# Kernel optimization log

Hardware: AMD Instinct MI355X
Metric: run time of the kernel (lower is better)

## Reference

```python
import jax, jax.numpy as jnp
import numpy as np

NUM_HEAD = 8


def setup_inputs() -> dict:
    key = jax.random.key(0)
    ks = jax.random.split(key, 8)
    B, N, M, C, R = 4, 2048, 2048, 256, 128
    s = 1.0 / np.sqrt(C)
    return {
        "input_q": jax.random.normal(ks[0], (B, N, C), jnp.float32),
        "input_k": jax.random.normal(ks[1], (B, M, C), jnp.float32),
        "input_v": jax.random.normal(ks[2], (B, M, C), jnp.float32),
        "rpe_indices": jax.random.randint(ks[3], (B, N, M), 0, R, jnp.int32),
        "key_masks": jnp.zeros((B, M), jnp.float32),
        "Wq": jax.random.normal(ks[4], (C, C), jnp.float32) * s,
        "bq": jnp.zeros((C,), jnp.float32),
        "Wk": jax.random.normal(ks[5], (C, C), jnp.float32) * s,
        "bk": jnp.zeros((C,), jnp.float32),
        "Wv": jax.random.normal(ks[6], (C, C), jnp.float32) * s,
        "bv": jnp.zeros((C,), jnp.float32),
        "rpe_bank": jax.random.normal(ks[7], (R, C), jnp.float32),
    }


def reference(input_q, input_k, input_v, rpe_indices, key_masks,
              Wq, bq, Wk, bk, Wv, bv, rpe_bank):
    B, N, C = input_q.shape
    M = input_k.shape[1]
    H = NUM_HEAD
    Dh = C // H
    R = rpe_bank.shape[0]

    # projections -> (B, H, len, Dh)
    q = (input_q @ Wq + bq).reshape(B, N, H, Dh).transpose(0, 2, 1, 3)
    k = (input_k @ Wk + bk).reshape(B, M, H, Dh).transpose(0, 2, 1, 3)
    v = (input_v @ Wv + bv).reshape(B, M, H, Dh).transpose(0, 2, 1, 3)

    # RPE bank split per head: (H, R, Dh)
    rpe = rpe_bank.reshape(R, H, Dh).transpose(1, 0, 2)

    # q . rpe for all bins, then gather per (n, m) relative index
    scores_p_all = jnp.einsum('bhnd,hrd->bhnr', q, rpe)            # (B,H,N,R)
    idx = jnp.broadcast_to(rpe_indices[:, None, :, :], (B, H, N, M))
    scores_p = jnp.take_along_axis(scores_p_all, idx, axis=-1)     # (B,H,N,M)

    scores_e = jnp.einsum('bhnd,bhmd->bhnm', q, k)                 # (B,H,N,M)
    scores = (scores_e + scores_p) / jnp.sqrt(jnp.asarray(Dh, q.dtype))
    scores = scores + key_masks[:, None, None, :]

    attn = jax.nn.softmax(scores, axis=-1)
    out = jnp.einsum('bhnm,bhmd->bhnd', attn, v)                   # (B,H,N,Dh)
    return out.transpose(0, 2, 1, 3).reshape(B, N, C)
```

## Files before the change

### kernel.cpp

```cpp
#include <hip/hip_runtime.h>
#include <hip/hip_bf16.h>

#define B_ 4
#define N_ 2048
#define M_ 2048
#define C_ 256
#define H_ 8
#define DH_ 32
#define R_ 128

typedef __bf16 bf16x8 __attribute__((ext_vector_type(8)));
typedef float f32x4 __attribute__((ext_vector_type(4)));

#define QSCL 0.25503486f
#define LOG2E 1.4426950408889634f
#define DTHR 11.5f

#define GLOAD_LDS4(gp, lp)                                            \
    __builtin_amdgcn_global_load_lds(                                 \
        (const __attribute__((address_space(1))) void*)(gp),          \
        (__attribute__((address_space(3))) void*)(lp), 4, 0, 0)

__global__ __launch_bounds__(256) void wtrans_kernel(
    const float* __restrict__ Wq, const float* __restrict__ Wk,
    const float* __restrict__ Wv, __bf16* __restrict__ out)
{
    __shared__ float t[32][33];
    int pz = blockIdx.z;
    const float* W = pz == 0 ? Wq : (pz == 1 ? Wk : Wv);
    int j0 = blockIdx.x * 32, k0 = blockIdx.y * 32;
    int tx = threadIdx.x, ty = threadIdx.y;
#pragma unroll
    for (int i = 0; i < 4; ++i)
        t[ty + 8 * i][tx] = W[(k0 + ty + 8 * i) * C_ + j0 + tx];
    __syncthreads();
    __bf16* o = out + (size_t)pz * C_ * C_;
#pragma unroll
    for (int i = 0; i < 4; ++i)
        o[(j0 + ty + 8 * i) * C_ + k0 + tx] = (__bf16)t[tx][ty + 8 * i];
}

__global__ __launch_bounds__(256) void proj_kernel(
    const float* __restrict__ Xq, const float* __restrict__ Xk, const float* __restrict__ Xv,
    const float* __restrict__ bq, const float* __restrict__ bk, const float* __restrict__ bv,
    const __bf16* __restrict__ Wt,
    __bf16* __restrict__ qb, __bf16* __restrict__ kb, __bf16* __restrict__ vt)
{
    int pz = blockIdx.z;
    const float* X = pz == 0 ? Xq : (pz == 1 ? Xk : Xv);
    const float* bias = pz == 0 ? bq : (pz == 1 ? bk : bv);
    const __bf16* W = Wt + (size_t)pz * C_ * C_;

    int r0 = blockIdx.x * 64;
    int w = threadIdx.x >> 6, lane = threadIdx.x & 63;
    int lg = lane >> 4, lr = lane & 15;
    int rw = r0 + w * 16;

    f32x4 z = {0.f, 0.f, 0.f, 0.f};
    f32x4 acc[16];
#pragma unroll
    for (int ns = 0; ns < 16; ++ns) acc[ns] = z;

    for (int ks = 0; ks < 8; ++ks) {
        const float* ap = X + (size_t)(rw + lr) * C_ + ks * 32 + lg * 8;
        float4 a0 = *(const float4*)ap;
        float4 a1 = *(const float4*)(ap + 4);
        bf16x8 af;
        af[0] = (__bf16)a0.x; af[1] = (__bf16)a0.y; af[2] = (__bf16)a0.z; af[3] = (__bf16)a0.w;
        af[4] = (__bf16)a1.x; af[5] = (__bf16)a1.y; af[6] = (__bf16)a1.z; af[7] = (__bf16)a1.w;
        if (pz < 2) {
#pragma unroll
            for (int ns = 0; ns < 16; ++ns) {
                bf16x8 bfv = *(const bf16x8*)(W + (size_t)(ns * 16 + lr) * C_ + ks * 32 + lg * 8);
                acc[ns] = __builtin_amdgcn_mfma_f32_16x16x32_bf16(bfv, af, acc[ns], 0, 0, 0);
            }
        } else {
#pragma unroll
            for (int ns = 0; ns < 16; ++ns) {
                bf16x8 bfv = *(const bf16x8*)(W + (size_t)(ns * 16 + lr) * C_ + ks * 32 + lg * 8);
                acc[ns] = __builtin_amdgcn_mfma_f32_16x16x32_bf16(af, bfv, acc[ns], 0, 0, 0);
            }
        }
    }

    if (pz < 2) {
        int ng = rw + lr;
        int bb = ng >> 11, n = ng & (N_ - 1);
        unsigned short* dst = (unsigned short*)(pz == 0 ? qb : kb);
#pragma unroll
        for (int ns = 0; ns < 16; ++ns) {
            int j0b = ns * 16 + 4 * lg;
            float4 b4 = *(const float4*)(bias + j0b);
            int hh = j0b >> 5, d0 = j0b & 31;
            float v0 = acc[ns][0] + b4.x, v1 = acc[ns][1] + b4.y;
            float v2 = acc[ns][2] + b4.z, v3 = acc[ns][3] + b4.w;
            if (pz == 0) { v0 *= QSCL; v1 *= QSCL; v2 *= QSCL; v3 *= QSCL; }
            ushort4 pk;
            pk.x = __builtin_bit_cast(unsigned short, (__bf16)v0);
            pk.y = __builtin_bit_cast(unsigned short, (__bf16)v1);
            pk.z = __builtin_bit_cast(unsigned short, (__bf16)v2);
            pk.w = __builtin_bit_cast(unsigned short, (__bf16)v3);
            *(ushort4*)(dst + ((((size_t)bb * H_ + hh) * 2048 + n) * DH_ + d0)) = pk;
        }
    } else {
        int r = rw + lg * 4;
        int bb = r >> 11, n = r & (N_ - 1);
#pragma unroll
        for (int ns = 0; ns < 16; ++ns) {
            int j = ns * 16 + lr;
            float bj = bias[j];
            int hh = j >> 5, d = j & 31;
            ushort4 pk;
            pk.x = __builtin_bit_cast(unsigned short, (__bf16)(acc[ns][0] + bj));
            pk.y = __builtin_bit_cast(unsigned short, (__bf16)(acc[ns][1] + bj));
            pk.z = __builtin_bit_cast(unsigned short, (__bf16)(acc[ns][2] + bj));
            pk.w = __builtin_bit_cast(unsigned short, (__bf16)(acc[ns][3] + bj));
            *(ushort4*)((unsigned short*)vt + (((size_t)bb * H_ + hh) * DH_ + d) * M_ + n) = pk;
        }
    }
}

__global__ __launch_bounds__(512) void attn_kernel(
    const __bf16* __restrict__ qb, const __bf16* __restrict__ kb,
    const __bf16* __restrict__ vt, const int* __restrict__ ridx,
    const float* __restrict__ kmask, const float* __restrict__ rbank,
    float* __restrict__ out)
{
    __shared__ __bf16 Pall[H_][16][R_];
    __shared__ int idxS[2][16 * 64];

    int lin = blockIdx.x;
    int b = (lin & 7) >> 1;
    int xq = ((lin >> 3) << 1) | (lin & 1);
    int n0 = xq * 16;

    int h = threadIdx.x >> 6, lane = threadIdx.x & 63;
    int lg = lane >> 4, lr = lane & 15;
    f32x4 z = {0.f, 0.f, 0.f, 0.f};

    const int* ixblk = ridx + ((size_t)b * N_ + n0) * M_;

#pragma unroll
    for (int i = 0; i < 2; ++i) {
        int r = 2 * h + i;
        int sw = 4 * (r & 7);
        GLOAD_LDS4(ixblk + (size_t)r * M_ + (lane ^ sw), &idxS[0][r * 64]);
    }

    bf16x8 qf = *(const bf16x8*)(qb + (((size_t)b * H_ + h) * N_ + n0 + lr) * DH_ + lg * 8);

    for (int rs = 0; rs < R_ / 16; ++rs) {
        const float* rp = rbank + (size_t)(rs * 16 + lr) * C_ + h * DH_ + lg * 8;
        float4 r0v = *(const float4*)rp;
        float4 r1v = *(const float4*)(rp + 4);
        bf16x8 rf;
        rf[0] = (__bf16)r0v.x; rf[1] = (__bf16)r0v.y; rf[2] = (__bf16)r0v.z; rf[3] = (__bf16)r0v.w;
        rf[4] = (__bf16)r1v.x; rf[5] = (__bf16)r1v.y; rf[6] = (__bf16)r1v.z; rf[7] = (__bf16)r1v.w;
        f32x4 pc = __builtin_amdgcn_mfma_f32_16x16x32_bf16(qf, rf, z, 0, 0, 0);
#pragma unroll
        for (int reg = 0; reg < 4; ++reg)
            Pall[h][lg * 4 + reg][rs * 16 + lr] = (__bf16)pc[reg];
    }

    __syncthreads();

    const __bf16* Kh = kb + ((size_t)b * H_ + h) * M_ * DH_;
    const __bf16* Vh = vt + ((size_t)b * H_ + h) * DH_ * M_;
    const float* km = kmask + (size_t)b * M_;
    const __bf16* PallR = &Pall[h][lr][0];
    int swzR = 4 * (lr & 7);

    float mrow = -1e30f, lrun = 0.f;
    f32x4 acc[2] = {z, z};
    int cb = 0;

    for (int mt = 0; mt < M_ / 64; ++mt) {
        int m0 = mt * 64;
        int m0n = (mt < 31) ? m0 + 64 : m0;

#pragma unroll
        for (int i = 0; i < 2; ++i) {
            int r = 2 * h + i;
            int sw = 4 * (r & 7);
            GLOAD_LDS4(ixblk + (size_t)r * M_ + m0n + (lane ^ sw), &idxS[cb ^ 1][r * 64]);
        }

        bf16x8 kf[4];
#pragma unroll
        for (int ms = 0; ms < 4; ++ms)
            kf[ms] = *(const bf16x8*)(Kh + (size_t)(m0 + ms * 16 + lr) * DH_ + lg * 8);
        bf16x8 vf[4];
#pragma unroll
        for (int ds = 0; ds < 2; ++ds)
#pragma unroll
            for (int ks = 0; ks < 2; ++ks)
                vf[ds * 2 + ks] = *(const bf16x8*)(Vh + (size_t)(ds * 16 + lr) * M_ + m0 + ks * 32 + lg * 8);
        float4 mkv[4];
#pragma unroll
        for (int ms = 0; ms < 4; ++ms)
            mkv[ms] = *(const float4*)(km + m0 + ms * 16 + 4 * lg);

        int4 ixv[4];
#pragma unroll
        for (int ms = 0; ms < 4; ++ms)
            ixv[ms] = *(const int4*)&idxS[cb][lr * 64 + ((16 * ms + 4 * lg) ^ swzR)];
        float sv[16];
#pragma unroll
        for (int ms = 0; ms < 4; ++ms) {
            sv[ms * 4 + 0] = (float)PallR[ixv[ms].x];
            sv[ms * 4 + 1] = (float)PallR[ixv[ms].y];
            sv[ms * 4 + 2] = (float)PallR[ixv[ms].z];
            sv[ms * 4 + 3] = (float)PallR[ixv[ms].w];
        }

        f32x4 st[4];
#pragma unroll
        for (int ms = 0; ms < 4; ++ms)
            st[ms] = __builtin_amdgcn_mfma_f32_16x16x32_bf16(kf[ms], qf, z, 0, 0, 0);

#pragma unroll
        for (int ms = 0; ms < 4; ++ms) {
            sv[ms * 4 + 0] = fmaf(mkv[ms].x, LOG2E, st[ms][0] + sv[ms * 4 + 0]);
            sv[ms * 4 + 1] = fmaf(mkv[ms].y, LOG2E, st[ms][1] + sv[ms * 4 + 1]);
            sv[ms * 4 + 2] = fmaf(mkv[ms].z, LOG2E, st[ms][2] + sv[ms * 4 + 2]);
            sv[ms * 4 + 3] = fmaf(mkv[ms].w, LOG2E, st[ms][3] + sv[ms * 4 + 3]);
        }

        float pmax = sv[0];
#pragma unroll
        for (int j = 1; j < 16; ++j) pmax = fmaxf(pmax, sv[j]);
        pmax = fmaxf(pmax, __shfl_xor(pmax, 16));
        pmax = fmaxf(pmax, __shfl_xor(pmax, 32));

        if (!__all(pmax - mrow <= DTHR)) {
            float mnew = fmaxf(mrow, pmax);
            float alpha = exp2f(mrow - mnew);
            mrow = mnew;
            lrun *= alpha;
#pragma unroll
            for (int reg = 0; reg < 4; ++reg) {
                float aB = __shfl(alpha, lg * 4 + reg);
                acc[0][reg] *= aB;
                acc[1][reg] *= aB;
            }
        }

        float pq[16], ssum = 0.f;
#pragma unroll
        for (int j = 0; j < 16; ++j) {
            pq[j] = exp2f(sv[j] - mrow);
            ssum += pq[j];
        }
        ssum += __shfl_xor(ssum, 16);
        ssum += __shfl_xor(ssum, 32);
        lrun += ssum;

        unsigned int pw[8];
#pragma unroll
        for (int p = 0; p < 8; ++p) {
            unsigned int lo = __builtin_bit_cast(unsigned short, (__bf16)pq[2 * p]);
            unsigned int hi = __builtin_bit_cast(unsigned short, (__bf16)pq[2 * p + 1]);
            pw[p] = lo | (hi << 16);
        }
        bool hiHalf = lane >= 32;
#pragma unroll
        for (int ks = 0; ks < 2; ++ks) {
            uint4 wv;
            unsigned int* wp = (unsigned int*)&wv;
#pragma unroll
            for (int wi = 0; wi < 4; ++wi) {
                int src = (((2 * lg + (wi >> 1)) & 3) << 4) + lr;
                unsigned int a0 = __shfl(pw[4 * ks + (wi & 1)], src);
                unsigned int a1 = __shfl(pw[4 * ks + 2 + (wi & 1)], src);
                wp[wi] = hiHalf ? a1 : a0;
            }
            bf16x8 pf = __builtin_bit_cast(bf16x8, wv);
#pragma unroll
            for (int ds = 0; ds < 2; ++ds)
                acc[ds] = __builtin_amdgcn_mfma_f32_16x16x32_bf16(pf, vf[ds * 2 + ks], acc[ds], 0, 0, 0);
        }

        __syncthreads();
        cb ^= 1;
    }

#pragma unroll
    for (int reg = 0; reg < 4; ++reg) {
        float lB = __shfl(lrun, lg * 4 + reg);
        float inv = 1.0f / lB;
        size_t rb = ((size_t)b * N_ + n0 + lg * 4 + reg) * C_ + h * DH_;
        out[rb + lr] = acc[0][reg] * inv;
        out[rb + 16 + lr] = acc[1][reg] * inv;
    }
}

extern "C" void kernel_launch(void* const* d_in, const int* in_sizes, int n_in,
                              void* d_out, int out_size, void* d_ws, size_t ws_size,
                              hipStream_t stream) {
    const float* Xq = (const float*)d_in[0];
    const float* Xk = (const float*)d_in[1];
    const float* Xv = (const float*)d_in[2];
    const int* ridx = (const int*)d_in[3];
    const float* kmask = (const float*)d_in[4];
    const float* Wq = (const float*)d_in[5];
    const float* bq = (const float*)d_in[6];
    const float* Wk = (const float*)d_in[7];
    const float* bk = (const float*)d_in[8];
    const float* Wv = (const float*)d_in[9];
    const float* bv = (const float*)d_in[10];
    const float* rbank = (const float*)d_in[11];
    float* outp = (float*)d_out;

    char* ws = (char*)d_ws;
    __bf16* Wt = (__bf16*)ws;
    __bf16* qb = (__bf16*)(ws + 393216);
    __bf16* kb = (__bf16*)(ws + 393216 + 4194304);
    __bf16* vt = (__bf16*)(ws + 393216 + 8388608);

    wtrans_kernel<<<dim3(8, 8, 3), dim3(32, 8), 0, stream>>>(Wq, Wk, Wv, Wt);
    proj_kernel<<<dim3(128, 1, 3), 256, 0, stream>>>(Xq, Xk, Xv, bq, bk, bv, Wt, qb, kb, vt);
    attn_kernel<<<512, 512, 0, stream>>>(qb, kb, vt, ridx, kmask, rbank, outp);
}
```

Before: 168.2 us.

## Split attention over key halves with a merge kernel and fast exp2

```diff
diff --git a/kernel.cpp b/kernel.cpp
--- a/kernel.cpp
+++ b/kernel.cpp
@@ -15,6 +15,12 @@
 #define QSCL 0.25503486f
 #define LOG2E 1.4426950408889634f
 #define DTHR 11.5f
+
+__device__ __forceinline__ float fast_exp2(float x) {
+    float r;
+    asm("v_exp_f32 %0, %1" : "=v"(r) : "v"(x));
+    return r;
+}
 
 #define GLOAD_LDS4(gp, lp)                                            \
     __builtin_amdgcn_global_load_lds(                                 \
@@ -120,19 +126,21 @@
     }
 }
 
-__global__ __launch_bounds__(512) void attn_kernel(
+__global__ __launch_bounds__(512, 8) void attn_kernel(
     const __bf16* __restrict__ qb, const __bf16* __restrict__ kb,
     const __bf16* __restrict__ vt, const int* __restrict__ ridx,
     const float* __restrict__ kmask, const float* __restrict__ rbank,
-    float* __restrict__ out)
+    float* __restrict__ Opart, float* __restrict__ Ms, float* __restrict__ Ls)
 {
     __shared__ __bf16 Pall[H_][16][R_];
     __shared__ int idxS[2][16 * 64];
 
     int lin = blockIdx.x;
+    int mh = lin & 1;
     int b = (lin & 7) >> 1;
-    int xq = ((lin >> 3) << 1) | (lin & 1);
+    int xq = lin >> 3;
     int n0 = xq * 16;
+    int mbase = mh * (M_ / 2);
 
     int h = threadIdx.x >> 6, lane = threadIdx.x & 63;
     int lg = lane >> 4, lr = lane & 15;
@@ -144,7 +152,7 @@
     for (int i = 0; i < 2; ++i) {
         int r = 2 * h + i;
         int sw = 4 * (r & 7);
-        GLOAD_LDS4(ixblk + (size_t)r * M_ + (lane ^ sw), &idxS[0][r * 64]);
+        GLOAD_LDS4(ixblk + (size_t)r * M_ + mbase + (lane ^ sw), &idxS[0][r * 64]);
     }
 
     bf16x8 qf = *(const bf16x8*)(qb + (((size_t)b * H_ + h) * N_ + n0 + lr) * DH_ + lg * 8);
@@ -174,9 +182,9 @@
     f32x4 acc[2] = {z, z};
     int cb = 0;
 
-    for (int mt = 0; mt < M_ / 64; ++mt) {
-        int m0 = mt * 64;
-        int m0n = (mt < 31) ? m0 + 64 : m0;
+    for (int mt = 0; mt < 16; ++mt) {
+        int m0 = mbase + mt * 64;
+        int m0n = (mt < 15) ? m0 + 64 : m0;
 
 #pragma unroll
         for (int i = 0; i < 2; ++i) {
@@ -234,7 +242,7 @@
 
         if (!__all(pmax - mrow <= DTHR)) {
             float mnew = fmaxf(mrow, pmax);
-            float alpha = exp2f(mrow - mnew);
+            float alpha = fast_exp2(mrow - mnew);
             mrow = mnew;
             lrun *= alpha;
 #pragma unroll
@@ -248,7 +256,7 @@
         float pq[16], ssum = 0.f;
 #pragma unroll
         for (int j = 0; j < 16; ++j) {
-            pq[j] = exp2f(sv[j] - mrow);
+            pq[j] = fast_exp2(sv[j] - mrow);
             ssum += pq[j];
         }
         ssum += __shfl_xor(ssum, 16);
@@ -284,14 +292,49 @@
         cb ^= 1;
     }
 
+    float* Op = Opart + ((((size_t)mh * B_ + b) * N_ + n0)) * C_ + h * DH_;
 #pragma unroll
     for (int reg = 0; reg < 4; ++reg) {
-        float lB = __shfl(lrun, lg * 4 + reg);
-        float inv = 1.0f / lB;
-        size_t rb = ((size_t)b * N_ + n0 + lg * 4 + reg) * C_ + h * DH_;
-        out[rb + lr] = acc[0][reg] * inv;
-        out[rb + 16 + lr] = acc[1][reg] * inv;
-    }
+        size_t rb = (size_t)(4 * lg + reg) * C_;
+        Op[rb + lr] = acc[0][reg];
+        Op[rb + 16 + lr] = acc[1][reg];
+    }
+    if (lane < 16) {
+        size_t si = (((size_t)mh * B_ + b) * H_ + h) * N_ + n0 + lr;
+        Ms[si] = mrow;
+        Ls[si] = lrun;
+    }
+}
+
+__global__ __launch_bounds__(256) void merge_kernel(
+    const float* __restrict__ Opart, const float* __restrict__ Ms,
+    const float* __restrict__ Ls, float* __restrict__ out)
+{
+    int t = blockIdx.x * 256 + threadIdx.x;
+    int c4 = t & 63;
+    int n = (t >> 6) & (N_ - 1);
+    int bb = t >> 17;
+    int h = c4 >> 3;
+
+    size_t s0 = ((size_t)bb * H_ + h) * N_ + n;
+    size_t s1 = (((size_t)B_ + bb) * H_ + h) * N_ + n;
+    float m0 = Ms[s0], m1 = Ms[s1];
+    float l0 = Ls[s0], l1 = Ls[s1];
+    float mm = fmaxf(m0, m1);
+    float w0 = fast_exp2(m0 - mm), w1 = fast_exp2(m1 - mm);
+    float inv = 1.0f / (l0 * w0 + l1 * w1);
+    w0 *= inv; w1 *= inv;
+
+    size_t o0i = ((size_t)bb * N_ + n) * C_ + c4 * 4;
+    size_t o1i = (((size_t)B_ + bb) * N_ + n) * C_ + c4 * 4;
+    float4 o0 = *(const float4*)(Opart + o0i);
+    float4 o1 = *(const float4*)(Opart + o1i);
+    float4 r;
+    r.x = o0.x * w0 + o1.x * w1;
+    r.y = o0.y * w0 + o1.y * w1;
+    r.z = o0.z * w0 + o1.z * w1;
+    r.w = o0.w * w0 + o1.w * w1;
+    *(float4*)(out + ((size_t)bb * N_ + n) * C_ + c4 * 4) = r;
 }
 
 extern "C" void kernel_launch(void* const* d_in, const int* in_sizes, int n_in,
@@ -316,8 +359,12 @@
     __bf16* qb = (__bf16*)(ws + 393216);
     __bf16* kb = (__bf16*)(ws + 393216 + 4194304);
     __bf16* vt = (__bf16*)(ws + 393216 + 8388608);
+    float* Opart = (float*)(ws + 12976128);
+    float* Msb = (float*)(ws + 12976128 + 16777216);
+    float* Lsb = (float*)(ws + 12976128 + 16777216 + 524288);
 
     wtrans_kernel<<<dim3(8, 8, 3), dim3(32, 8), 0, stream>>>(Wq, Wk, Wv, Wt);
     proj_kernel<<<dim3(128, 1, 3), 256, 0, stream>>>(Xq, Xk, Xv, bq, bk, bv, Wt, qb, kb, vt);
-    attn_kernel<<<512, 512, 0, stream>>>(qb, kb, vt, ridx, kmask, rbank, outp);
-}
+    attn_kernel<<<1024, 512, 0, stream>>>(qb, kb, vt, ridx, kmask, rbank, Opart, Msb, Lsb);
+    merge_kernel<<<2048, 256, 0, stream>>>(Opart, Msb, Lsb, outp);
+}
```

Measured after the change: 207.0 us. 1.23x slower.

## Permute V layout to drop P shuffles, prefetch K, defer row-sum reduction

Applied to the files above, without the earlier changes.

```diff
diff --git a/kernel.cpp b/kernel.cpp
--- a/kernel.cpp
+++ b/kernel.cpp
@@ -15,6 +15,12 @@
 #define QSCL 0.25503486f
 #define LOG2E 1.4426950408889634f
 #define DTHR 11.5f
+
+__device__ __forceinline__ float fast_exp2(float x) {
+    float r;
+    asm("v_exp_f32 %0, %1" : "=v"(r) : "v"(x));
+    return r;
+}
 
 #define GLOAD_LDS4(gp, lp)                                            \
     __builtin_amdgcn_global_load_lds(                                 \
@@ -105,6 +111,7 @@
     } else {
         int r = rw + lg * 4;
         int bb = r >> 11, n = r & (N_ - 1);
+        int np = (n & ~31) | (((n >> 2) & 3) << 3) | (((n >> 4) & 1) << 2);
 #pragma unroll
         for (int ns = 0; ns < 16; ++ns) {
             int j = ns * 16 + lr;
@@ -115,12 +122,12 @@
             pk.y = __builtin_bit_cast(unsigned short, (__bf16)(acc[ns][1] + bj));
             pk.z = __builtin_bit_cast(unsigned short, (__bf16)(acc[ns][2] + bj));
             pk.w = __builtin_bit_cast(unsigned short, (__bf16)(acc[ns][3] + bj));
-            *(ushort4*)((unsigned short*)vt + (((size_t)bb * H_ + hh) * DH_ + d) * M_ + n) = pk;
-        }
-    }
-}
-
-__global__ __launch_bounds__(512) void attn_kernel(
+            *(ushort4*)((unsigned short*)vt + (((size_t)bb * H_ + hh) * DH_ + d) * M_ + np) = pk;
+        }
+    }
+}
+
+__global__ __launch_bounds__(512, 4) void attn_kernel(
     const __bf16* __restrict__ qb, const __bf16* __restrict__ kb,
     const __bf16* __restrict__ vt, const int* __restrict__ ridx,
     const float* __restrict__ kmask, const float* __restrict__ rbank,
@@ -162,18 +169,24 @@
             Pall[h][lg * 4 + reg][rs * 16 + lr] = (__bf16)pc[reg];
     }
 
-    __syncthreads();
-
     const __bf16* Kh = kb + ((size_t)b * H_ + h) * M_ * DH_;
     const __bf16* Vh = vt + ((size_t)b * H_ + h) * DH_ * M_;
     const float* km = kmask + (size_t)b * M_;
     const __bf16* PallR = &Pall[h][lr][0];
     int swzR = 4 * (lr & 7);
 
-    float mrow = -1e30f, lrun = 0.f;
+    bf16x8 kf[4];
+#pragma unroll
+    for (int ms = 0; ms < 4; ++ms)
+        kf[ms] = *(const bf16x8*)(Kh + (size_t)(ms * 16 + lr) * DH_ + lg * 8);
+
+    __syncthreads();
+
+    float mrow = -1e30f, lloc = 0.f;
     f32x4 acc[2] = {z, z};
     int cb = 0;
 
+#pragma unroll 2
     for (int mt = 0; mt < M_ / 64; ++mt) {
         int m0 = mt * 64;
         int m0n = (mt < 31) ? m0 + 64 : m0;
@@ -185,10 +198,11 @@
             GLOAD_LDS4(ixblk + (size_t)r * M_ + m0n + (lane ^ sw), &idxS[cb ^ 1][r * 64]);
         }
 
-        bf16x8 kf[4];
+        bf16x8 kf_n[4];
 #pragma unroll
         for (int ms = 0; ms < 4; ++ms)
-            kf[ms] = *(const bf16x8*)(Kh + (size_t)(m0 + ms * 16 + lr) * DH_ + lg * 8);
+            kf_n[ms] = *(const bf16x8*)(Kh + (size_t)(m0n + ms * 16 + lr) * DH_ + lg * 8);
+
         bf16x8 vf[4];
 #pragma unroll
         for (int ds = 0; ds < 2; ++ds)
@@ -226,17 +240,19 @@
             sv[ms * 4 + 3] = fmaf(mkv[ms].w, LOG2E, st[ms][3] + sv[ms * 4 + 3]);
         }
 
-        float pmax = sv[0];
-#pragma unroll
-        for (int j = 1; j < 16; ++j) pmax = fmaxf(pmax, sv[j]);
-        pmax = fmaxf(pmax, __shfl_xor(pmax, 16));
-        pmax = fmaxf(pmax, __shfl_xor(pmax, 32));
+        float t0 = fmaxf(fmaxf(sv[0], sv[1]), fmaxf(sv[2], sv[3]));
+        float t1 = fmaxf(fmaxf(sv[4], sv[5]), fmaxf(sv[6], sv[7]));
+        float t2 = fmaxf(fmaxf(sv[8], sv[9]), fmaxf(sv[10], sv[11]));
+        float t3 = fmaxf(fmaxf(sv[12], sv[13]), fmaxf(sv[14], sv[15]));
+        float pmax = fmaxf(fmaxf(t0, t1), fmaxf(t2, t3));
 
         if (!__all(pmax - mrow <= DTHR)) {
-            float mnew = fmaxf(mrow, pmax);
-            float alpha = exp2f(mrow - mnew);
+            float rmax = fmaxf(pmax, __shfl_xor(pmax, 16));
+            rmax = fmaxf(rmax, __shfl_xor(rmax, 32));
+            float mnew = fmaxf(mrow, rmax);
+            float alpha = fast_exp2(mrow - mnew);
             mrow = mnew;
-            lrun *= alpha;
+            lloc *= alpha;
 #pragma unroll
             for (int reg = 0; reg < 4; ++reg) {
                 float aB = __shfl(alpha, lg * 4 + reg);
@@ -245,36 +261,22 @@
             }
         }
 
-        float pq[16], ssum = 0.f;
-#pragma unroll
-        for (int j = 0; j < 16; ++j) {
-            pq[j] = exp2f(sv[j] - mrow);
-            ssum += pq[j];
-        }
-        ssum += __shfl_xor(ssum, 16);
-        ssum += __shfl_xor(ssum, 32);
-        lrun += ssum;
-
-        unsigned int pw[8];
-#pragma unroll
-        for (int p = 0; p < 8; ++p) {
-            unsigned int lo = __builtin_bit_cast(unsigned short, (__bf16)pq[2 * p]);
-            unsigned int hi = __builtin_bit_cast(unsigned short, (__bf16)pq[2 * p + 1]);
-            pw[p] = lo | (hi << 16);
-        }
-        bool hiHalf = lane >= 32;
+        float pq[16];
+#pragma unroll
+        for (int j = 0; j < 16; ++j) pq[j] = fast_exp2(sv[j] - mrow);
+        {
+            float s0 = (pq[0] + pq[1]) + (pq[2] + pq[3]);
+            float s1 = (pq[4] + pq[5]) + (pq[6] + pq[7]);
+            float s2 = (pq[8] + pq[9]) + (pq[10] + pq[11]);
+            float s3 = (pq[12] + pq[13]) + (pq[14] + pq[15]);
+            lloc += (s0 + s1) + (s2 + s3);
+        }
+
 #pragma unroll
         for (int ks = 0; ks < 2; ++ks) {
-            uint4 wv;
-            unsigned int* wp = (unsigned int*)&wv;
-#pragma unroll
-            for (int wi = 0; wi < 4; ++wi) {
-                int src = (((2 * lg + (wi >> 1)) & 3) << 4) + lr;
-                unsigned int a0 = __shfl(pw[4 * ks + (wi & 1)], src);
-                unsigned int a1 = __shfl(pw[4 * ks + 2 + (wi & 1)], src);
-                wp[wi] = hiHalf ? a1 : a0;
-            }
-            bf16x8 pf = __builtin_bit_cast(bf16x8, wv);
+            bf16x8 pf;
+#pragma unroll
+            for (int e = 0; e < 8; ++e) pf[e] = (__bf16)pq[8 * ks + e];
 #pragma unroll
             for (int ds = 0; ds < 2; ++ds)
                 acc[ds] = __builtin_amdgcn_mfma_f32_16x16x32_bf16(pf, vf[ds * 2 + ks], acc[ds], 0, 0, 0);
@@ -282,11 +284,15 @@
 
         __syncthreads();
         cb ^= 1;
-    }
-
+#pragma unroll
+        for (int ms = 0; ms < 4; ++ms) kf[ms] = kf_n[ms];
+    }
+
+    float lrow = lloc + __shfl_xor(lloc, 16);
+    lrow += __shfl_xor(lrow, 32);
 #pragma unroll
     for (int reg = 0; reg < 4; ++reg) {
-        float lB = __shfl(lrun, lg * 4 + reg);
+        float lB = __shfl(lrow, lg * 4 + reg);
         float inv = 1.0f / lB;
         size_t rb = ((size_t)b * N_ + n0 + lg * 4 + reg) * C_ + h * DH_;
         out[rb + lr] = acc[0][reg] * inv;
```

New measurement: 171.7 us. 1.02x slower.
